# Optimization experiments

Measured on AMD Instinct MI355X. Metric: run time of the kernel, lower is better.

Reference implementation:

```python
import math
import jax, jax.numpy as jnp
import numpy as np

B, N, D = 16, 2048, 256
EPS = 1e-8  # torch cosine_similarity default eps
TAU = 3.0   # gumbel-softmax temperature


def setup_inputs() -> dict:
    key = jax.random.key(0)
    k1, k2 = jax.random.split(key)
    return {
        "LowLevelFeatures": jax.random.normal(k1, (B, 1, N, D), dtype=jnp.float32),
        "HighLevelFeatures": jax.random.normal(k2, (B, 1, N, D), dtype=jnp.float32),
        "batch_size": B,
    }


def _forward(LLF4, HLF4):
    LLF = LLF4[:, 0]  # [B,N,D]
    HLF = HLF4[:, 0]  # [B,N,D]
    b, n, d = LLF.shape
    # pairwise cosine similarity [B,N,N]: matmul + norm-product (same math as
    # torch's broadcast cosine_similarity, without the [B,N,N,D] intermediate)
    dots = jnp.einsum('bnd,bmd->bnm', LLF, HLF)
    nl = jnp.linalg.norm(LLF, axis=-1)  # [B,N]
    nh = jnp.linalg.norm(HLF, axis=-1)  # [B,N]
    sim = dots / jnp.maximum(nl[:, :, None] * nh[:, None, :], EPS)
    sim = sim / math.sqrt(d)
    probs = jax.nn.softmax(sim, axis=1)  # softmax over dim 1 (LLF rows)
    # F.gumbel_softmax(probs, tau=3, hard=True, dim=1): probs act as logits
    u = jax.random.uniform(jax.random.key(42), probs.shape,
                           minval=1e-10, maxval=1.0)
    gumbels = -jnp.log(-jnp.log(u))
    y_soft = jax.nn.softmax((probs + gumbels) / TAU, axis=1)
    idx = jnp.argmax(y_soft, axis=1)  # [B,N]: selected LLF-row n per HLF col m
    # torch.where on the one-hot scans row-major over (b, n, m), so per batch
    # the returned n-indices are the SORTED multiset of selected indices
    sl = jnp.sort(idx, axis=-1)  # [B,N]
    bidx = jnp.arange(b)[:, None]  # [B,1]
    aligned = HLF[bidx, sl]  # gather along dim 1 -> [B,N,D]
    # rowwise cosine similarity between gathered HLF and LLF
    w = jnp.sum(aligned * LLF, axis=-1) / jnp.maximum(
        jnp.linalg.norm(aligned, axis=-1) * nl, EPS)  # [B,N]
    noise = jax.nn.softmax(w / 0.1, axis=1)[:, :, None]  # [B,N,1]
    hlf_new = aligned + LLF * noise
    out = HLF.at[bidx, sl].set(hlf_new)
    return out


def reference(LowLevelFeatures, HighLevelFeatures, batch_size):
    return _forward(LowLevelFeatures, HighLevelFeatures)
```

## Files before the change

kernel.cpp:

```cpp
#include <hip/hip_runtime.h>
#include <math.h>

#define NB 16
#define NN 2048
#define ND 256
#define BNtot (NB*NN)
#define HH 33554432u

typedef __attribute__((ext_vector_type(8))) short bf16x8;
typedef __attribute__((ext_vector_type(4))) float f32x4;

__device__ __forceinline__ void gld16(const void* g, void* l){
  __builtin_amdgcn_global_load_lds((const __attribute__((address_space(1))) void*)g,
                                   (__attribute__((address_space(3))) void*)l, 16, 0, 0);
}

__device__ __forceinline__ unsigned rotl(unsigned v, int r){
  return __builtin_amdgcn_alignbit(v, v, 32-r);
}
__device__ __forceinline__ unsigned umaxu(unsigned a, unsigned b){ return a > b ? a : b; }
__device__ __forceinline__ unsigned uminu(unsigned a, unsigned b){ return a < b ? a : b; }

__device__ __forceinline__ float gumbelv(unsigned b, unsigned n, unsigned m){
  unsigned f = (b<<22) | (n<<11) | m;
  unsigned x0 = (b < 8u) ? f : (f - HH);
  unsigned x1 = x0 + HH;
  const unsigned ks0=0u, ks1=42u, ks2=0u^42u^0x1BD11BDAu;
  unsigned v0 = x0 + ks0;
  unsigned v1 = x1 + ks1;
#define TFR(r) { v0 += v1; v1 = rotl(v1,(r)); v1 ^= v0; }
  TFR(13) TFR(15) TFR(26) TFR(6)
  v0 += ks1; v1 += ks2 + 1u;
  TFR(17) TFR(29) TFR(16) TFR(24)
  v0 += ks2; v1 += ks0 + 2u;
  TFR(13) TFR(15) TFR(26) TFR(6)
  v0 += ks0; v1 += ks1 + 3u;
  TFR(17) TFR(29) TFR(16) TFR(24)
  v0 += ks1; v1 += ks2 + 4u;
  TFR(13) TFR(15) TFR(26) TFR(6)
  v0 += ks2; v1 += ks0 + 5u;
#undef TFR
  unsigned bits = (b < 8u) ? v0 : v1;
  float fl = __uint_as_float((bits>>9) | 0x3F800000u) - 1.0f;
  float u = fmaxf(1e-10f, fl + 1e-10f);
  return -logf(-logf(u));
}

__device__ __forceinline__ float gfromkey(unsigned key){
  float fl = __uint_as_float(key | 0x3F800000u) - 1.0f;
  float u = fmaxf(1e-10f, fl + 1e-10f);
  return -logf(-logf(u));
}

struct GumState {
  unsigned x0, vk, a1, a2, c1, c2;
  int t;
};

__device__ __forceinline__ void gum_init(GumState& g, int gb){
  g.t = gb*256 + (int)threadIdx.x;
  int half = g.t & 1;
  int m    = (g.t >> 1) & 2047;
  int bl   = (g.t >> 12) & 7;
  int nq   = g.t >> 15;
  int nstart = (nq << 7) + (half << 6);
  g.x0 = ((unsigned)bl << 22) | ((unsigned)nstart << 11) | (unsigned)m;
  g.a1 = g.a2 = g.c1 = g.c2 = 0;
  g.vk = (unsigned)(127 - (half<<6));
}

__device__ __forceinline__ void gum_iter(GumState& g, const int cnt){
  const unsigned KS2 = 42u ^ 0x1BD11BDAu;
  unsigned x0=g.x0, vk=g.vk, a1=g.a1, a2=g.a2, c1=g.c1, c2=g.c2;
#define TFR(r)       { v0 += v1; v1 = rotl(v1,(r)); v1 ^= v0; }
#define TFRI(r, inj) { v0 += v1 + (inj); v1 = rotl(v1,(r)); v1 ^= v0; }
  #pragma unroll 4
  for (int j = 0; j < cnt; ++j){
    unsigned v0 = x0;
    unsigned v1 = x0 + (HH + 42u);
    TFR(13) TFR(15) TFR(26) TFR(6)
    v1 += KS2 + 1u;
    TFRI(17, 42u) TFR(29) TFR(16) TFR(24)
    v1 += 2u;
    TFRI(13, KS2) TFR(15) TFR(26) TFR(6)
    v1 += 42u + 3u;
    TFR(17) TFR(29) TFR(16) TFR(24)
    v1 += KS2 + 4u;
    TFRI(13, 42u) TFR(15) TFR(26) TFR(6)
    v0 += KS2; v1 += 5u;
    unsigned pa = (v0 & 0xFFFFFE00u) | vk;
    unsigned pb = (v1 & 0xFFFFFE00u) | vk;
    unsigned ta = uminu(pa, a1);
    a1 = umaxu(pa, a1);
    a2 = umaxu(ta, a2);
    unsigned tc = uminu(pb, c1);
    c1 = umaxu(pb, c1);
    c2 = umaxu(tc, c2);
    x0 += 2048u;
    vk -= 1u;
  }
#undef TFR
#undef TFRI
  g.x0=x0; g.vk=vk; g.a1=a1; g.a2=a2; g.c1=c1; g.c2=c2;
}

__device__ __forceinline__ void gum_finish(const GumState& g, float* __restrict__ pcv,
                                           int* __restrict__ pci){
  int half = g.t & 1;
  int m    = (g.t >> 1) & 2047;
  int bl   = (g.t >> 12) & 7;
  int nq   = g.t >> 15;
  int chunkbase = nq << 7;
  unsigned p1 = __shfl_xor((int)g.a1, 1), p2 = __shfl_xor((int)g.a2, 1);
  unsigned q1 = __shfl_xor((int)g.c1, 1), q2 = __shfl_xor((int)g.c2, 1);
  unsigned A1 = umaxu(g.a1, p1);
  unsigned A2 = umaxu(uminu(g.a1, p1), umaxu(g.a2, p2));
  unsigned C1 = umaxu(g.c1, q1);
  unsigned C2 = umaxu(uminu(g.c1, q1), umaxu(g.c2, q2));
  if (half == 0){
    int baseA = (((nq*NB + bl  )*NN + m) << 1);
    int baseB = (((nq*NB + bl+8)*NN + m) << 1);
    pcv[baseA+0] = gfromkey(A1 >> 9); pci[baseA+0] = chunkbase + 127 - (int)(A1 & 127u);
    pcv[baseA+1] = gfromkey(A2 >> 9); pci[baseA+1] = chunkbase + 127 - (int)(A2 & 127u);
    pcv[baseB+0] = gfromkey(C1 >> 9); pci[baseB+0] = chunkbase + 127 - (int)(C1 & 127u);
    pcv[baseB+1] = gfromkey(C2 >> 9); pci[baseB+1] = chunkbase + 127 - (int)(C2 & 127u);
  }
}

__launch_bounds__(256)
__global__ void kgumbel(float* __restrict__ pcv, int* __restrict__ pci){
  GumState g; gum_init(g, blockIdx.x);
  gum_iter(g, 64);
  gum_finish(g, pcv, pci);
}

__device__ __forceinline__ void prep_rows(const float4* v, int wid, int lane,
                                          ushort* __restrict__ dst, float* __restrict__ nrm){
  #pragma unroll
  for (int i=0;i<4;i++){
    int row = wid*4 + i;
    float s = v[i].x*v[i].x + v[i].y*v[i].y + v[i].z*v[i].z + v[i].w*v[i].w;
    for (int o=32;o;o>>=1) s += __shfl_down(s,o);
    if (lane==0) nrm[row] = sqrtf(s);
    uint2 u;
    u.x = (__float_as_uint(v[i].y)&0xFFFF0000u)|(__float_as_uint(v[i].x)>>16);
    u.y = (__float_as_uint(v[i].w)&0xFFFF0000u)|(__float_as_uint(v[i].z)>>16);
    int b = row >> 11, nloc = row & 2047;
    int k = lane << 2;
    int ck = k >> 6;
    int j  = k & 63;
    int qi = j >> 3;
    size_t off = (size_t)b*524288 + (size_t)ck*131072 + (size_t)nloc*64
               + ((qi ^ (nloc & 7)) << 3) + (j & 7);
    *(uint2*)(dst + off) = u;
  }
}

__global__ void knorms(const float* __restrict__ LLF, const float* __restrict__ HLF,
                       float* __restrict__ nl, float* __restrict__ nh){
  int row = blockIdx.x;
  int wave = threadIdx.x >> 6;
  int lane = threadIdx.x & 63;
  const float* src = wave ? HLF : LLF;
  float4 v = ((const float4*)(src + (size_t)row*ND))[lane];
  float s = v.x*v.x + v.y*v.y + v.z*v.z + v.w*v.w;
  for (int o=32;o;o>>=1) s += __shfl_down(s,o);
  if (lane==0) (wave? nh: nl)[row] = sqrtf(s);
}

__launch_bounds__(256, 8)
__global__ void kfuse1(const float* __restrict__ LLF, const float* __restrict__ HLF,
                       ushort* __restrict__ Abf, ushort* __restrict__ Bbf,
                       float* __restrict__ nl, float* __restrict__ nh,
                       float* __restrict__ pcv, int* __restrict__ pci){
  int t = blockIdx.x*256 + (int)threadIdx.x;
  int wid = t >> 6;
  int lane = t & 63;
  GumState g; gum_init(g, blockIdx.x);
  float4 va[4];
  #pragma unroll
  for (int i=0;i<4;i++)
    va[i] = ((const float4*)(LLF + (size_t)(wid*4+i)*ND))[lane];
  gum_iter(g, 32);
  prep_rows(va, wid, lane, Abf, nl);
  float4 vb[4];
  #pragma unroll
  for (int i=0;i<4;i++)
    vb[i] = ((const float4*)(HLF + (size_t)(wid*4+i)*ND))[lane];
  gum_iter(g, 32);
  prep_rows(vb, wid, lane, Bbf, nh);
  gum_finish(g, pcv, pci);
}

#define K1 0.09016844f
__launch_bounds__(256)
__global__ void kgemm_dma(const ushort* __restrict__ Abf, const ushort* __restrict__ Bbf,
                          const float* __restrict__ nl, const float* __restrict__ nh,
                          float* __restrict__ partS){
  __shared__ ushort As[128*64];
  __shared__ ushort Bs[128*64];
  __shared__ float colsum[128];
  const int b  = blockIdx.z;
  const int n0 = blockIdx.y << 7;
  const int m0 = blockIdx.x << 7;
  const int tid  = threadIdx.x;
  const int lane = tid & 63;
  const int w    = tid >> 6;
  const int wn   = w >> 1, wm = w & 1;
  const int quad = lane >> 4, l15 = lane & 15;
  if (tid < 128) colsum[tid] = 0.0f;

  const ushort* Ab = Abf + (size_t)b*524288;
  const ushort* Bb = Bbf + (size_t)b*524288;

  f32x4 acc[4][4];
  #pragma unroll
  for (int i=0;i<4;i++)
    #pragma unroll
    for (int j=0;j<4;j++) acc[i][j] = (f32x4){0.f,0.f,0.f,0.f};

  for (int ck=0; ck<4; ck++){
    __syncthreads();
    const ushort* ga = Ab + (size_t)ck*131072 + (size_t)n0*64;
    const ushort* gb = Bb + (size_t)ck*131072 + (size_t)m0*64;
    #pragma unroll
    for (int t=0;t<4;t++){
      int seg = (w*4 + t) * 512;
      gld16(ga + seg + lane*8, &As[seg]);
      gld16(gb + seg + lane*8, &Bs[seg]);
    }
    __syncthreads();
    #pragma unroll
    for (int ks=0; ks<64; ks+=32){
      bf16x8 af[4], bf[4];
      #pragma unroll
      for (int t=0;t<4;t++){
        int R = wn*64 + t*16 + l15;
        af[t] = *(const bf16x8*)(&As[R*64 + ((((ks>>3)+quad) ^ (R&7))<<3)]);
      }
      #pragma unroll
      for (int t=0;t<4;t++){
        int R = wm*64 + t*16 + l15;
        bf[t] = *(const bf16x8*)(&Bs[R*64 + ((((ks>>3)+quad) ^ (R&7))<<3)]);
      }
      #pragma unroll
      for (int ti=0;ti<4;ti++)
        #pragma unroll
        for (int tj=0;tj<4;tj++)
          acc[ti][tj] = __builtin_amdgcn_mfma_f32_16x16x32_bf16(af[ti], bf[tj], acc[ti][tj], 0, 0, 0);
    }
  }

  float an[4][4];
  #pragma unroll
  for (int ti=0;ti<4;ti++)
    #pragma unroll
    for (int r=0;r<4;r++)
      an[ti][r] = K1 / nl[b*NN + n0 + wn*64 + ti*16 + quad*4 + r];
  float bm[4];
  #pragma unroll
  for (int tj=0;tj<4;tj++)
    bm[tj] = 1.0f / nh[b*NN + m0 + wm*64 + tj*16 + l15];
  #pragma unroll
  for (int tj=0;tj<4;tj++){
    float s = 0.0f;
    #pragma unroll
    for (int ti=0;ti<4;ti++)
      #pragma unroll
      for (int r=0;r<4;r++)
        s += __builtin_amdgcn_exp2f(acc[ti][tj][r]*an[ti][r]*bm[tj] - K1);
    s += __shfl_down(s, 32);
    s += __shfl_down(s, 16);
    if (lane < 16) atomicAdd(&colsum[wm*64 + tj*16 + l15], s);
  }
  __syncthreads();
  if (tid < 128)
    partS[(size_t)blockIdx.y*BNtot + b*NN + m0 + tid] = colsum[tid];
}

__launch_bounds__(256)
__global__ void kgemm_mfma(const float* __restrict__ LLF, const float* __restrict__ HLF,
                           const float* __restrict__ nl, const float* __restrict__ nh,
                           float* __restrict__ partS){
  __shared__ ushort As[128][72];
  __shared__ ushort Bs[128][72];
  __shared__ float colsum[128];
  const int b  = blockIdx.z;
  const int n0 = blockIdx.y << 7;
  const int m0 = blockIdx.x << 7;
  const float* Ab = LLF + (size_t)b*NN*ND;
  const float* Bb = HLF + (size_t)b*NN*ND;
  const int tid  = threadIdx.x;
  const int lane = tid & 63;
  const int w    = tid >> 6;
  const int wn   = w >> 1, wm = w & 1;
  const int quad = lane >> 4, l15 = lane & 15;
  if (tid < 128) colsum[tid] = 0.0f;

  f32x4 acc[4][4];
  #pragma unroll
  for (int i=0;i<4;i++)
    #pragma unroll
    for (int j=0;j<4;j++) acc[i][j] = (f32x4){0.f,0.f,0.f,0.f};

  const int rbase = tid >> 3;
  const int kq    = (tid & 7) << 3;

  for (int ck=0; ck<4; ck++){
    const int k0 = ck << 6;
    __syncthreads();
    #pragma unroll
    for (int pi=0; pi<4; pi++){
      int row = rbase + (pi<<5);
      const float* pa = Ab + (size_t)(n0+row)*ND + k0 + kq;
      float4 a0 = *(const float4*)pa;
      float4 a1 = *(const float4*)(pa+4);
      uint4 ua;
      ua.x = (__float_as_uint(a0.y)&0xFFFF0000u)|(__float_as_uint(a0.x)>>16);
      ua.y = (__float_as_uint(a0.w)&0xFFFF0000u)|(__float_as_uint(a0.z)>>16);
      ua.z = (__float_as_uint(a1.y)&0xFFFF0000u)|(__float_as_uint(a1.x)>>16);
      ua.w = (__float_as_uint(a1.w)&0xFFFF0000u)|(__float_as_uint(a1.z)>>16);
      *(uint4*)(&As[row][kq]) = ua;
      const float* pb = Bb + (size_t)(m0+row)*ND + k0 + kq;
      float4 b0 = *(const float4*)pb;
      float4 b1 = *(const float4*)(pb+4);
      uint4 ub;
      ub.x = (__float_as_uint(b0.y)&0xFFFF0000u)|(__float_as_uint(b0.x)>>16);
      ub.y = (__float_as_uint(b0.w)&0xFFFF0000u)|(__float_as_uint(b0.z)>>16);
      ub.z = (__float_as_uint(b1.y)&0xFFFF0000u)|(__float_as_uint(b1.x)>>16);
      ub.w = (__float_as_uint(b1.w)&0xFFFF0000u)|(__float_as_uint(b1.z)>>16);
      *(uint4*)(&Bs[row][kq]) = ub;
    }
    __syncthreads();
    #pragma unroll
    for (int ks=0; ks<64; ks+=32){
      bf16x8 af[4], bf[4];
      #pragma unroll
      for (int t=0;t<4;t++)
        af[t] = *(const bf16x8*)(&As[wn*64 + t*16 + l15][ks + quad*8]);
      #pragma unroll
      for (int t=0;t<4;t++)
        bf[t] = *(const bf16x8*)(&Bs[wm*64 + t*16 + l15][ks + quad*8]);
      #pragma unroll
      for (int ti=0;ti<4;ti++)
        #pragma unroll
        for (int tj=0;tj<4;tj++)
          acc[ti][tj] = __builtin_amdgcn_mfma_f32_16x16x32_bf16(af[ti], bf[tj], acc[ti][tj], 0, 0, 0);
    }
  }

  float an[4][4];
  #pragma unroll
  for (int ti=0;ti<4;ti++)
    #pragma unroll
    for (int r=0;r<4;r++)
      an[ti][r] = K1 / nl[b*NN + n0 + wn*64 + ti*16 + quad*4 + r];
  float bm[4];
  #pragma unroll
  for (int tj=0;tj<4;tj++)
    bm[tj] = 1.0f / nh[b*NN + m0 + wm*64 + tj*16 + l15];
  #pragma unroll
  for (int tj=0;tj<4;tj++){
    float s = 0.0f;
    #pragma unroll
    for (int ti=0;ti<4;ti++)
      #pragma unroll
      for (int r=0;r<4;r++)
        s += __builtin_amdgcn_exp2f(acc[ti][tj][r]*an[ti][r]*bm[tj] - K1);
    s += __shfl_down(s, 32);
    s += __shfl_down(s, 16);
    if (lane < 16) atomicAdd(&colsum[wm*64 + tj*16 + l15], s);
  }
  __syncthreads();
  if (tid < 128)
    partS[(size_t)blockIdx.y*BNtot + b*NN + m0 + tid] = colsum[tid];
}

__launch_bounds__(256)
__global__ void kresolve(const float* __restrict__ LLF, const float* __restrict__ HLF,
                         const float* __restrict__ nl, const float* __restrict__ nh,
                         const float* __restrict__ partS,
                         const float* __restrict__ pcv, const int* __restrict__ pci,
                         int* __restrict__ idx){
  int w    = threadIdx.x >> 6;
  int lane = threadIdx.x & 63;
  int g = blockIdx.x*4 + w;
  int b = g >> 11, m = g & 2047;
  float ps = (lane < 16) ? partS[(size_t)lane*BNtot + g] : 0.0f;
  ps += __shfl_down(ps, 8);
  ps += __shfl_down(ps, 4);
  ps += __shfl_down(ps, 2);
  ps += __shfl_down(ps, 1);
  float invS = 1.0f / __shfl(ps, 0);
  float pv = -INFINITY; int pn = 0;
  if (lane < 32){
    int base = ((((lane>>1)*NB + b)*NN + m) << 1) + (lane & 1);
    pv = pcv[base]; pn = pci[base];
  }
  float gmax = pv;
  for (int o=32;o;o>>=1) gmax = fmaxf(gmax, __shfl_down(gmax,o));
  gmax = __shfl(gmax, 0);
  unsigned long long mask = __ballot(pv >= gmax - 8e-5f);
  mask &= 0xFFFFFFFFull;
  float4 h = ((const float4*)(HLF + (size_t)g*ND))[lane];
  float nhg = nh[g];
  float bestQ = -INFINITY; int bestN = 1<<30;
  while (mask){
    int src = __builtin_ctzll(mask); mask &= mask-1;
    int   n  = __shfl(pn, src);
    float gv = __shfl(pv, src);
    float4 a = ((const float4*)(LLF + ((size_t)b*NN + n)*ND))[lane];
    float d = a.x*h.x + a.y*h.y + a.z*h.z + a.w*h.w;
    for (int o=32;o;o>>=1) d += __shfl_down(d,o);
    d = __shfl(d, 0);
    float sim = (d / fmaxf(nl[b*NN+n]*nhg, 1e-8f)) * 0.0625f;
    float q = expf(sim - 0.0625f)*invS + gv;
    if (q > bestQ || (q == bestQ && n < bestN)){ bestQ = q; bestN = n; }
  }
  if (lane==0) idx[g] = bestN;
}

__launch_bounds__(256)
__global__ void kstats(const float* __restrict__ A, const float* __restrict__ Bm,
                       const float* __restrict__ nl, const float* __restrict__ nh,
                       float* __restrict__ Mout, float* __restrict__ Sinv){
  __shared__ float As[64][33];
  __shared__ float Bs[64][33];
  __shared__ float Cs[64][65];
  const int b  = blockIdx.x >> 5;
  const int m0 = (blockIdx.x & 31) << 6;
  const float* Ab = A  + (size_t)b*NN*ND;
  const float* Bb = Bm + (size_t)b*NN*ND;
  const int tid = threadIdx.x;
  const int tx = tid & 15, ty = tid >> 4;
  float nhv[4];
  #pragma unroll
  for (int j=0;j<4;j++) nhv[j] = nh[b*NN + m0 + tx*4 + j];
  float Mr = -INFINITY, Sr = 0.0f;
  for (int nt=0; nt<NN; nt+=64){
    float acc[4][4] = {{0.f,0.f,0.f,0.f},{0.f,0.f,0.f,0.f},{0.f,0.f,0.f,0.f},{0.f,0.f,0.f,0.f}};
    for (int kc=0; kc<ND; kc+=32){
      __syncthreads();
      #pragma unroll
      for (int s=0;s<2;s++){
        int f = tid + (s<<8);
        int r = f >> 3;
        int c = (f & 7) << 2;
        float4 va = *(const float4*)(Ab + (size_t)(nt+r)*ND + kc + c);
        As[r][c]=va.x; As[r][c+1]=va.y; As[r][c+2]=va.z; As[r][c+3]=va.w;
        float4 vb = *(const float4*)(Bb + (size_t)(m0+r)*ND + kc + c);
        Bs[r][c]=vb.x; Bs[r][c+1]=vb.y; Bs[r][c+2]=vb.z; Bs[r][c+3]=vb.w;
      }
      __syncthreads();
      #pragma unroll 4
      for (int k=0;k<32;k++){
        float a0=As[ty*4+0][k], a1=As[ty*4+1][k], a2=As[ty*4+2][k], a3=As[ty*4+3][k];
        float b0=Bs[tx*4+0][k], b1=Bs[tx*4+1][k], b2=Bs[tx*4+2][k], b3=Bs[tx*4+3][k];
        acc[0][0]+=a0*b0; acc[0][1]+=a0*b1; acc[0][2]+=a0*b2; acc[0][3]+=a0*b3;
        acc[1][0]+=a1*b0; acc[1][1]+=a1*b1; acc[1][2]+=a1*b2; acc[1][3]+=a1*b3;
        acc[2][0]+=a2*b0; acc[2][1]+=a2*b1; acc[2][2]+=a2*b2; acc[2][3]+=a2*b3;
        acc[3][0]+=a3*b0; acc[3][1]+=a3*b1; acc[3][2]+=a3*b2; acc[3][3]+=a3*b3;
      }
    }
    float nlv[4];
    #pragma unroll
    for (int i=0;i<4;i++) nlv[i] = nl[b*NN + nt + ty*4 + i];
    __syncthreads();
    #pragma unroll
    for (int i=0;i<4;i++)
      #pragma unroll
      for (int j=0;j<4;j++){
        float denom = fmaxf(nlv[i]*nhv[j], 1e-8f);
        Cs[ty*4+i][tx*4+j] = (acc[i][j]/denom)*0.0625f;
      }
    __syncthreads();
    if (tid < 64){
      float tmax = -INFINITY;
      #pragma unroll 8
      for (int r=0;r<64;r++) tmax = fmaxf(tmax, Cs[r][tid]);
      float newM = fmaxf(Mr, tmax);
      float s = 0.0f;
      #pragma unroll 4
      for (int r=0;r<64;r++) s += expf(Cs[r][tid]-newM);
      Sr = Sr*expf(Mr-newM) + s;
      Mr = newM;
    }
  }
  if (tid < 64){
    Mout[b*NN+m0+tid] = Mr;
    Sinv[b*NN+m0+tid] = 1.0f/Sr;
  }
}

__launch_bounds__(256)
__global__ void kargmax(const float* __restrict__ A, const float* __restrict__ Bm,
                        const float* __restrict__ nl, const float* __restrict__ nh,
                        const float* __restrict__ Mv, const float* __restrict__ Sv,
                        int* __restrict__ idxout){
  __shared__ float As[64][33];
  __shared__ float Bs[64][33];
  __shared__ float Vs[16][64];
  __shared__ int   Is[16][64];
  const int b  = blockIdx.x >> 5;
  const int m0 = (blockIdx.x & 31) << 6;
  const float* Ab = A  + (size_t)b*NN*ND;
  const float* Bb = Bm + (size_t)b*NN*ND;
  const int tid = threadIdx.x;
  const int tx = tid & 15, ty = tid >> 4;
  float nhv[4], Mj[4], iSj[4];
  #pragma unroll
  for (int j=0;j<4;j++){
    int m = m0 + tx*4 + j;
    nhv[j] = nh[b*NN + m];
    Mj[j]  = Mv[b*NN + m];
    iSj[j] = Sv[b*NN + m];
  }
  float bestV = -INFINITY; int bestN = 0;
  for (int nt=0; nt<NN; nt+=64){
    float acc[4][4] = {{0.f,0.f,0.f,0.f},{0.f,0.f,0.f,0.f},{0.f,0.f,0.f,0.f},{0.f,0.f,0.f,0.f}};
    for (int kc=0; kc<ND; kc+=32){
      __syncthreads();
      #pragma unroll
      for (int s=0;s<2;s++){
        int f = tid + (s<<8);
        int r = f >> 3;
        int c = (f & 7) << 2;
        float4 va = *(const float4*)(Ab + (size_t)(nt+r)*ND + kc + c);
        As[r][c]=va.x; As[r][c+1]=va.y; As[r][c+2]=va.z; As[r][c+3]=va.w;
        float4 vb = *(const float4*)(Bb + (size_t)(m0+r)*ND + kc + c);
        Bs[r][c]=vb.x; Bs[r][c+1]=vb.y; Bs[r][c+2]=vb.z; Bs[r][c+3]=vb.w;
      }
      __syncthreads();
      #pragma unroll 4
      for (int k=0;k<32;k++){
        float a0=As[ty*4+0][k], a1=As[ty*4+1][k], a2=As[ty*4+2][k], a3=As[ty*4+3][k];
        float b0=Bs[tx*4+0][k], b1=Bs[tx*4+1][k], b2=Bs[tx*4+2][k], b3=Bs[tx*4+3][k];
        acc[0][0]+=a0*b0; acc[0][1]+=a0*b1; acc[0][2]+=a0*b2; acc[0][3]+=a0*b3;
        acc[1][0]+=a1*b0; acc[1][1]+=a1*b1; acc[1][2]+=a1*b2; acc[1][3]+=a1*b3;
        acc[2][0]+=a2*b0; acc[2][1]+=a2*b1; acc[2][2]+=a2*b2; acc[2][3]+=a2*b3;
        acc[3][0]+=a3*b0; acc[3][1]+=a3*b1; acc[3][2]+=a3*b2; acc[3][3]+=a3*b3;
      }
    }
    float nlv[4];
    #pragma unroll
    for (int i=0;i<4;i++) nlv[i] = nl[b*NN + nt + ty*4 + i];
    float lv[4]; int li[4];
    #pragma unroll
    for (int j=0;j<4;j++){ lv[j] = -INFINITY; li[j] = 0; }
    #pragma unroll
    for (int i=0;i<4;i++){
      int n = nt + ty*4 + i;
      #pragma unroll
      for (int j=0;j<4;j++){
        float denom = fmaxf(nlv[i]*nhv[j], 1e-8f);
        float sim = (acc[i][j]/denom)*0.0625f;
        float p = expf(sim - Mj[j]) * iSj[j];
        float v = p + gumbelv((unsigned)b, (unsigned)n, (unsigned)(m0 + tx*4 + j));
        if (v > lv[j]) { lv[j] = v; li[j] = n; }
      }
    }
    __syncthreads();
    #pragma unroll
    for (int j=0;j<4;j++){ Vs[ty][tx*4+j]=lv[j]; Is[ty][tx*4+j]=li[j]; }
    __syncthreads();
    if (tid < 64){
      #pragma unroll 4
      for (int t=0;t<16;t++){
        float v = Vs[t][tid];
        if (v > bestV){ bestV = v; bestN = Is[t][tid]; }
      }
    }
  }
  if (tid < 64) idxout[b*NN + m0 + tid] = bestN;
}

__global__ void ksort(const int* __restrict__ idx, int* __restrict__ cntg,
                      int* __restrict__ offg, int* __restrict__ sl){
  __shared__ int c[NN];
  __shared__ int part[256];
  int b = blockIdx.x, tid = threadIdx.x;
  for (int v=tid; v<NN; v+=256) c[v]=0;
  __syncthreads();
  for (int j=tid; j<NN; j+=256) atomicAdd(&c[idx[b*NN+j]], 1);
  __syncthreads();
  int base = tid*8, s=0, lc[8];
  #pragma unroll
  for (int k=0;k<8;k++){ lc[k]=c[base+k]; s+=lc[k]; }
  part[tid]=s; __syncthreads();
  for (int o=1;o<256;o<<=1){
    int v = (tid>=o)? part[tid-o] : 0;
    __syncthreads();
    part[tid]+=v;
    __syncthreads();
  }
  int run = part[tid]-s;
  #pragma unroll
  for (int k=0;k<8;k++){
    int v = base+k;
    cntg[b*NN+v]=lc[k];
    offg[b*NN+v]=run;
    for (int j=0;j<lc[k];j++) sl[b*NN+run+j]=v;
    run += lc[k];
  }
}

__global__ void kw(const float* __restrict__ LLF, const float* __restrict__ HLF,
                   const float* __restrict__ nl, const float* __restrict__ nh,
                   const int* __restrict__ sl, float* __restrict__ w){
  int g = blockIdx.x*4 + (threadIdx.x>>6);
  int lane = threadIdx.x & 63;
  int b = g >> 11;
  int s = sl[g];
  float4 a = ((const float4*)(HLF + ((size_t)b*NN + s)*ND))[lane];
  float4 l = ((const float4*)(LLF + (size_t)g*ND))[lane];
  float d = a.x*l.x + a.y*l.y + a.z*l.z + a.w*l.w;
  for (int o=32;o;o>>=1) d += __shfl_down(d,o);
  if (lane==0){
    float denom = fmaxf(nh[b*NN+s]*nl[g], 1e-8f);
    w[g] = d/denom;
  }
}

__global__ void knoise(const float* __restrict__ w, float* __restrict__ nz){
  int b = blockIdx.x, tid = threadIdx.x;
  __shared__ float sred[4];
  float x[8]; float mx = -INFINITY;
  #pragma unroll
  for (int k=0;k<8;k++){ x[k] = w[b*NN + tid*8 + k] / 0.1f; mx = fmaxf(mx, x[k]); }
  for (int o=32;o;o>>=1) mx = fmaxf(mx, __shfl_down(mx,o));
  mx = __shfl(mx, 0);
  if ((tid&63)==0) sred[tid>>6] = mx;
  __syncthreads();
  mx = fmaxf(fmaxf(sred[0],sred[1]), fmaxf(sred[2],sred[3]));
  __syncthreads();
  float e[8]; float s = 0.f;
  #pragma unroll
  for (int k=0;k<8;k++){ e[k] = expf(x[k]-mx); s += e[k]; }
  for (int o=32;o;o>>=1) s += __shfl_down(s,o);
  s = __shfl(s, 0);
  if ((tid&63)==0) sred[tid>>6] = s;
  __syncthreads();
  s = sred[0]+sred[1]+sred[2]+sred[3];
  #pragma unroll
  for (int k=0;k<8;k++) nz[b*NN + tid*8 + k] = e[k]/s;
}

__global__ void kfinal(const float* __restrict__ LLF, const float* __restrict__ HLF,
                       const int* __restrict__ cnt, const int* __restrict__ off,
                       const float* __restrict__ nz, float* __restrict__ out){
  int row = blockIdx.x;
  int lane = threadIdx.x;
  int b = row >> 11;
  float4 h = ((const float4*)(HLF + (size_t)row*ND))[lane];
  int c = cnt[row];
  if (c > 0){
    int i = off[row] + c - 1;
    float ns = nz[b*NN + i];
    float4 l = ((const float4*)(LLF + ((size_t)(b*NN + i))*ND))[lane];
    h.x += l.x*ns; h.y += l.y*ns; h.z += l.z*ns; h.w += l.w*ns;
  }
  ((float4*)(out + (size_t)row*ND))[lane] = h;
}

extern "C" void kernel_launch(void* const* d_in, const int* in_sizes, int n_in,
                              void* d_out, int out_size, void* d_ws, size_t ws_size,
                              hipStream_t stream){
  const float* LLF = (const float*)d_in[0];
  const float* HLF = (const float*)d_in[1];
  float* out = (float*)d_out;
  float* ws = (float*)d_ws;

  float* nl  = ws;
  float* nh  = ws + 1*(size_t)BNtot;
  float* iS  = ws + 2*(size_t)BNtot;
  int*   idx = (int*)(ws + 3*(size_t)BNtot);
  int*   cnt = (int*)(ws + 4*(size_t)BNtot);
  int*   off = (int*)(ws + 5*(size_t)BNtot);
  int*   sl  = (int*)(ws + 6*(size_t)BNtot);
  float* wv  = ws + 7*(size_t)BNtot;
  float* nz  = ws + 8*(size_t)BNtot;
  float* partS = ws + 9*(size_t)BNtot;
  float* pcv   = partS + 16*(size_t)BNtot;
  int*   pci   = (int*)(pcv + 32*(size_t)BNtot);
  ushort* Abf  = (ushort*)(pci + 32*(size_t)BNtot);
  ushort* Bbf  = Abf + (size_t)BNtot*ND;
  const size_t needBytes1 = (9 + 16 + 32 + 32) * (size_t)BNtot * 4;
  const size_t needBytes2 = needBytes1 + 2 * (size_t)BNtot * ND * 2;

  if (ws_size >= needBytes2){
    hipLaunchKernelGGL(kfuse1,  dim3(2048),      dim3(256), 0, stream, LLF, HLF, Abf, Bbf, nl, nh, pcv, pci);
    hipLaunchKernelGGL(kgemm_dma,dim3(16,16,16), dim3(256), 0, stream, Abf, Bbf, nl, nh, partS);
    hipLaunchKernelGGL(kresolve,dim3(BNtot/4),   dim3(256), 0, stream, LLF, HLF, nl, nh, partS, pcv, pci, idx);
  } else if (ws_size >= needBytes1){
    hipLaunchKernelGGL(knorms,   dim3(BNtot),      dim3(128), 0, stream, LLF, HLF, nl, nh);
    hipLaunchKernelGGL(kgemm_mfma,dim3(16,16,16),  dim3(256), 0, stream, LLF, HLF, nl, nh, partS);
    hipLaunchKernelGGL(kgumbel,  dim3(2048),       dim3(256), 0, stream, pcv, pci);
    hipLaunchKernelGGL(kresolve, dim3(BNtot/4),    dim3(256), 0, stream, LLF, HLF, nl, nh, partS, pcv, pci, idx);
  } else {
    float* Mv = ws + 9*(size_t)BNtot;
    hipLaunchKernelGGL(knorms,   dim3(BNtot),      dim3(128), 0, stream, LLF, HLF, nl, nh);
    hipLaunchKernelGGL(kstats,   dim3(NB*32),      dim3(256), 0, stream, LLF, HLF, nl, nh, Mv, iS);
    hipLaunchKernelGGL(kargmax,  dim3(NB*32),      dim3(256), 0, stream, LLF, HLF, nl, nh, Mv, iS, idx);
  }

  hipLaunchKernelGGL(ksort,  dim3(NB),      dim3(256), 0, stream, idx, cnt, off, sl);
  hipLaunchKernelGGL(kw,     dim3(BNtot/4), dim3(256), 0, stream, LLF, HLF, nl, nh, sl, wv);
  hipLaunchKernelGGL(knoise, dim3(NB),      dim3(256), 0, stream, wv, nz);
  hipLaunchKernelGGL(kfinal, dim3(BNtot),   dim3(64),  0, stream, LLF, HLF, cnt, off, nz, out);
}
```

Before: 284.0 us.

## Split Gumbel generation between prep kernel and GEMM waves, store packed keys

```diff
diff --git a/kernel.cpp b/kernel.cpp
--- a/kernel.cpp
+++ b/kernel.cpp
@@ -57,16 +57,21 @@
   int t;
 };
 
-__device__ __forceinline__ void gum_init(GumState& g, int gb){
-  g.t = gb*256 + (int)threadIdx.x;
-  int half = g.t & 1;
-  int m    = (g.t >> 1) & 2047;
-  int bl   = (g.t >> 12) & 7;
-  int nq   = g.t >> 15;
+__device__ __forceinline__ void gum_init(GumState& g, int t){
+  g.t = t;
+  int half = t & 1;
+  int m    = (t >> 1) & 2047;
+  int bl   = (t >> 12) & 7;
+  int nq   = t >> 15;
   int nstart = (nq << 7) + (half << 6);
   g.x0 = ((unsigned)bl << 22) | ((unsigned)nstart << 11) | (unsigned)m;
   g.a1 = g.a2 = g.c1 = g.c2 = 0;
   g.vk = (unsigned)(127 - (half<<6));
+}
+
+__device__ __forceinline__ void gum_seek(GumState& g, int o){
+  g.x0 += (unsigned)o * 2048u;
+  g.vk -= (unsigned)o;
 }
 
 __device__ __forceinline__ void gum_iter(GumState& g, const int cnt){
@@ -104,13 +109,12 @@
   g.x0=x0; g.vk=vk; g.a1=a1; g.a2=a2; g.c1=c1; g.c2=c2;
 }
 
-__device__ __forceinline__ void gum_finish(const GumState& g, float* __restrict__ pcv,
-                                           int* __restrict__ pci){
+__device__ __forceinline__ void gum_finish(const GumState& g, unsigned* __restrict__ pck,
+                                           int seg){
   int half = g.t & 1;
   int m    = (g.t >> 1) & 2047;
   int bl   = (g.t >> 12) & 7;
   int nq   = g.t >> 15;
-  int chunkbase = nq << 7;
   unsigned p1 = __shfl_xor((int)g.a1, 1), p2 = __shfl_xor((int)g.a2, 1);
   unsigned q1 = __shfl_xor((int)g.c1, 1), q2 = __shfl_xor((int)g.c2, 1);
   unsigned A1 = umaxu(g.a1, p1);
@@ -118,20 +122,22 @@
   unsigned C1 = umaxu(g.c1, q1);
   unsigned C2 = umaxu(uminu(g.c1, q1), umaxu(g.c2, q2));
   if (half == 0){
-    int baseA = (((nq*NB + bl  )*NN + m) << 1);
-    int baseB = (((nq*NB + bl+8)*NN + m) << 1);
-    pcv[baseA+0] = gfromkey(A1 >> 9); pci[baseA+0] = chunkbase + 127 - (int)(A1 & 127u);
-    pcv[baseA+1] = gfromkey(A2 >> 9); pci[baseA+1] = chunkbase + 127 - (int)(A2 & 127u);
-    pcv[baseB+0] = gfromkey(C1 >> 9); pci[baseB+0] = chunkbase + 127 - (int)(C1 & 127u);
-    pcv[baseB+1] = gfromkey(C2 >> 9); pci[baseB+1] = chunkbase + 127 - (int)(C2 & 127u);
+    size_t base = ((size_t)((nq<<2) + (seg<<1))*NB + bl)*NN + m;
+    pck[base]                 = A1;
+    pck[base + (size_t)BNtot] = A2;
+    pck[base + 8*NN]                 = C1;
+    pck[base + 8*NN + (size_t)BNtot] = C2;
   }
 }
 
 __launch_bounds__(256)
-__global__ void kgumbel(float* __restrict__ pcv, int* __restrict__ pci){
-  GumState g; gum_init(g, blockIdx.x);
-  gum_iter(g, 64);
-  gum_finish(g, pcv, pci);
+__global__ void kgumbel(unsigned* __restrict__ pck){
+  GumState g; gum_init(g, blockIdx.x*256 + (int)threadIdx.x);
+  gum_iter(g, 32);
+  gum_finish(g, pck, 0);
+  g.a1 = g.a2 = g.c1 = g.c2 = 0;
+  gum_iter(g, 32);
+  gum_finish(g, pck, 1);
 }
 
 __device__ __forceinline__ void prep_rows(const float4* v, int wid, int lane,
@@ -172,31 +178,31 @@
 __global__ void kfuse1(const float* __restrict__ LLF, const float* __restrict__ HLF,
                        ushort* __restrict__ Abf, ushort* __restrict__ Bbf,
                        float* __restrict__ nl, float* __restrict__ nh,
-                       float* __restrict__ pcv, int* __restrict__ pci){
+                       unsigned* __restrict__ pck){
   int t = blockIdx.x*256 + (int)threadIdx.x;
   int wid = t >> 6;
   int lane = t & 63;
-  GumState g; gum_init(g, blockIdx.x);
+  GumState g; gum_init(g, t);
   float4 va[4];
   #pragma unroll
   for (int i=0;i<4;i++)
     va[i] = ((const float4*)(LLF + (size_t)(wid*4+i)*ND))[lane];
-  gum_iter(g, 32);
+  gum_iter(g, 16);
   prep_rows(va, wid, lane, Abf, nl);
   float4 vb[4];
   #pragma unroll
   for (int i=0;i<4;i++)
     vb[i] = ((const float4*)(HLF + (size_t)(wid*4+i)*ND))[lane];
-  gum_iter(g, 32);
+  gum_iter(g, 16);
   prep_rows(vb, wid, lane, Bbf, nh);
-  gum_finish(g, pcv, pci);
+  gum_finish(g, pck, 0);
 }
 
 #define K1 0.09016844f
 __launch_bounds__(256)
 __global__ void kgemm_dma(const ushort* __restrict__ Abf, const ushort* __restrict__ Bbf,
                           const float* __restrict__ nl, const float* __restrict__ nh,
-                          float* __restrict__ partS){
+                          float* __restrict__ partS, unsigned* __restrict__ pck){
   __shared__ ushort As[128*64];
   __shared__ ushort Bs[128*64];
   __shared__ float colsum[128];
@@ -210,6 +216,14 @@
   const int quad = lane >> 4, l15 = lane & 15;
   if (tid < 128) colsum[tid] = 0.0f;
 
+  const int blockflat = (blockIdx.z*16 + (int)blockIdx.y)*16 + (int)blockIdx.x;
+  const bool gw = (w < 2);
+  GumState gs;
+  if (gw){
+    gum_init(gs, (blockflat*2 + w)*64 + lane);
+    gum_seek(gs, 32);
+  }
+
   const ushort* Ab = Abf + (size_t)b*524288;
   const ushort* Bb = Bbf + (size_t)b*524288;
 
@@ -229,6 +243,7 @@
       gld16(ga + seg + lane*8, &As[seg]);
       gld16(gb + seg + lane*8, &Bs[seg]);
     }
+    if (gw) gum_iter(gs, 8);
     __syncthreads();
     #pragma unroll
     for (int ks=0; ks<64; ks+=32){
@@ -276,6 +291,7 @@
   __syncthreads();
   if (tid < 128)
     partS[(size_t)blockIdx.y*BNtot + b*NN + m0 + tid] = colsum[tid];
+  if (gw) gum_finish(gs, pck, 1);
 }
 
 __launch_bounds__(256)
@@ -380,28 +396,25 @@
 __global__ void kresolve(const float* __restrict__ LLF, const float* __restrict__ HLF,
                          const float* __restrict__ nl, const float* __restrict__ nh,
                          const float* __restrict__ partS,
-                         const float* __restrict__ pcv, const int* __restrict__ pci,
+                         const unsigned* __restrict__ pck,
                          int* __restrict__ idx){
   int w    = threadIdx.x >> 6;
   int lane = threadIdx.x & 63;
   int g = blockIdx.x*4 + w;
-  int b = g >> 11, m = g & 2047;
+  int b = g >> 11;
   float ps = (lane < 16) ? partS[(size_t)lane*BNtot + g] : 0.0f;
   ps += __shfl_down(ps, 8);
   ps += __shfl_down(ps, 4);
   ps += __shfl_down(ps, 2);
   ps += __shfl_down(ps, 1);
   float invS = 1.0f / __shfl(ps, 0);
-  float pv = -INFINITY; int pn = 0;
-  if (lane < 32){
-    int base = ((((lane>>1)*NB + b)*NN + m) << 1) + (lane & 1);
-    pv = pcv[base]; pn = pci[base];
-  }
+  unsigned pk = pck[(size_t)lane*BNtot + g];
+  float pv = gfromkey(pk >> 9);
+  int   pn = ((lane >> 2) << 7) + 127 - (int)(pk & 127u);
   float gmax = pv;
   for (int o=32;o;o>>=1) gmax = fmaxf(gmax, __shfl_down(gmax,o));
   gmax = __shfl(gmax, 0);
   unsigned long long mask = __ballot(pv >= gmax - 8e-5f);
-  mask &= 0xFFFFFFFFull;
   float4 h = ((const float4*)(HLF + (size_t)g*ND))[lane];
   float nhg = nh[g];
   float bestQ = -INFINITY; int bestN = 1<<30;
@@ -680,22 +693,21 @@
   float* wv  = ws + 7*(size_t)BNtot;
   float* nz  = ws + 8*(size_t)BNtot;
   float* partS = ws + 9*(size_t)BNtot;
-  float* pcv   = partS + 16*(size_t)BNtot;
-  int*   pci   = (int*)(pcv + 32*(size_t)BNtot);
-  ushort* Abf  = (ushort*)(pci + 32*(size_t)BNtot);
+  unsigned* pck = (unsigned*)(ws + 25*(size_t)BNtot);
+  ushort* Abf  = (ushort*)(ws + 89*(size_t)BNtot);
   ushort* Bbf  = Abf + (size_t)BNtot*ND;
-  const size_t needBytes1 = (9 + 16 + 32 + 32) * (size_t)BNtot * 4;
+  const size_t needBytes1 = (9 + 16 + 64) * (size_t)BNtot * 4;
   const size_t needBytes2 = needBytes1 + 2 * (size_t)BNtot * ND * 2;
 
   if (ws_size >= needBytes2){
-    hipLaunchKernelGGL(kfuse1,  dim3(2048),      dim3(256), 0, stream, LLF, HLF, Abf, Bbf, nl, nh, pcv, pci);
-    hipLaunchKernelGGL(kgemm_dma,dim3(16,16,16), dim3(256), 0, stream, Abf, Bbf, nl, nh, partS);
-    hipLaunchKernelGGL(kresolve,dim3(BNtot/4),   dim3(256), 0, stream, LLF, HLF, nl, nh, partS, pcv, pci, idx);
+    hipLaunchKernelGGL(kfuse1,  dim3(2048),      dim3(256), 0, stream, LLF, HLF, Abf, Bbf, nl, nh, pck);
+    hipLaunchKernelGGL(kgemm_dma,dim3(16,16,16), dim3(256), 0, stream, Abf, Bbf, nl, nh, partS, pck);
+    hipLaunchKernelGGL(kresolve,dim3(BNtot/4),   dim3(256), 0, stream, LLF, HLF, nl, nh, partS, pck, idx);
   } else if (ws_size >= needBytes1){
     hipLaunchKernelGGL(knorms,   dim3(BNtot),      dim3(128), 0, stream, LLF, HLF, nl, nh);
     hipLaunchKernelGGL(kgemm_mfma,dim3(16,16,16),  dim3(256), 0, stream, LLF, HLF, nl, nh, partS);
-    hipLaunchKernelGGL(kgumbel,  dim3(2048),       dim3(256), 0, stream, pcv, pci);
-    hipLaunchKernelGGL(kresolve, dim3(BNtot/4),    dim3(256), 0, stream, LLF, HLF, nl, nh, partS, pcv, pci, idx);
+    hipLaunchKernelGGL(kgumbel,  dim3(2048),       dim3(256), 0, stream, pck);
+    hipLaunchKernelGGL(kresolve, dim3(BNtot/4),    dim3(256), 0, stream, LLF, HLF, nl, nh, partS, pck, idx);
   } else {
     float* Mv = ws + 9*(size_t)BNtot;
     hipLaunchKernelGGL(knorms,   dim3(BNtot),      dim3(128), 0, stream, LLF, HLF, nl, nh);
```

Result: slower. 311.4 us (+9.6%).
